# Optimization experiments

Hardware: AMD Instinct MI355X
Metric: run time of the kernel (lower is better)

Reference implementation:

```python
import jax, jax.numpy as jnp
import numpy as np


def _gaussian_splat_map(mask, sigma_x, sigma_y):
    """Equivalent to the torch scatter loop: for every pixel (p,q) with mask>0,
    add exp(-((i-p)^2/(2 sx^2) + (j-q)^2/(2 sy^2))) into map[b]. Because the
    Gaussian is separable, the sum over sources is exactly Gx @ M @ Gy with
    full HxH / WxW Gaussian distance kernels. Then normalize by per-batch max
    (max==0 -> 1)."""
    B, H, W = mask.shape
    ih = jnp.arange(H, dtype=jnp.float32)
    iw = jnp.arange(W, dtype=jnp.float32)
    dx = ih[:, None] - ih[None, :]                      # (H, H): i - p
    dy = iw[:, None] - iw[None, :]                      # (W, W): q - j (symmetric)
    Gx = jnp.exp(-(dx * dx) / (2.0 * sigma_x * sigma_x))
    Gy = jnp.exp(-(dy * dy) / (2.0 * sigma_y * sigma_y))
    m = (mask > 0).astype(jnp.float32)                  # (B, H, W) source indicator
    g = jnp.einsum('ip,bpq,qj->bij', Gx, m, Gy)         # summed Gaussians per batch
    mx = jnp.max(g, axis=(1, 2), keepdims=True)
    mx = jnp.where(mx == 0, jnp.float32(1.0), mx)
    return g / mx


def setup_inputs() -> dict:
    key = jax.random.key(0)
    B, C, H, W = 64, 4, 256, 256
    x = jax.random.normal(key, (B, C, H, W), dtype=jnp.float32)
    return {"x": x}


def reference(x):
    # x: (B, 4, H, W) -> output: (B, 5, H, W) with history=True, mul=True
    ch0 = x[:, 0, :, :]
    target = _gaussian_splat_map(x[:, 2, :, :], 1.0, 1.0)
    cost = _gaussian_splat_map(x[:, 1, :, :], 1.0, 1.0)
    hist = _gaussian_splat_map(x[:, 3, :, :], 0.5, 0.5)
    mul = target * cost
    return jnp.stack([ch0, target, cost, hist, mul], axis=1)
```

## Files before the change

kernel.cpp:

```cpp
#include <hip/hip_runtime.h>
#include <cmath>

#define HH 256
#define WW 256
#define BB 64
#define RR 4
#define OROWS 16
#define TROWS (OROWS + 2*RR)
#define TSTR 260

static __device__ __forceinline__ float bin(float v) { return (v > 0.0f) ? 1.0f : 0.0f; }

__global__ __launch_bounds__(256) void splat_kernel(const float* __restrict__ x,
                                                    float* __restrict__ out,
                                                    float* __restrict__ maxws) {
    __shared__ float tmp[TROWS * TSTR];
    __shared__ float wred[4];

    const int strip = blockIdx.x;
    const int z = blockIdx.y;
    const int b = z / 3;
    const int m = z - 3 * b;
    const int src_c = (m == 0) ? 2 : ((m == 1) ? 1 : 3);
    const float inv2s2 = (m == 2) ? 2.0f : 0.5f;

    float w[RR + 1];
#pragma unroll
    for (int d = 0; d <= RR; ++d) w[d] = expf(-(float)(d * d) * inv2s2);

    const int ti0 = strip * OROWS;
    const float* xc = x + (((size_t)b * 4 + src_c) << 16);
    const int tid = threadIdx.x;

#pragma unroll
    for (int t = 0; t < 3; ++t) {
        int idx = tid + t * 256;
        int r = idx >> 5;
        int g = idx & 31;
        int gi = ti0 + r - RR;
        float4 q0 = make_float4(0.f,0.f,0.f,0.f), q1 = q0, q2 = q0, q3 = q0;
        if (gi >= 0 && gi < HH) {
            const float4* row = (const float4*)(xc + ((size_t)gi << 8));
            int i0 = (g > 0) ? (2 * g - 1) : 0;
            int i3 = (g < 31) ? (2 * g + 2) : 63;
            q0 = row[i0];
            q1 = row[2 * g];
            q2 = row[2 * g + 1];
            q3 = row[i3];
            if (g == 0)  q0 = make_float4(0.f,0.f,0.f,0.f);
            if (g == 31) q3 = make_float4(0.f,0.f,0.f,0.f);
        }
        float a[16] = {bin(q0.x), bin(q0.y), bin(q0.z), bin(q0.w),
                       bin(q1.x), bin(q1.y), bin(q1.z), bin(q1.w),
                       bin(q2.x), bin(q2.y), bin(q2.z), bin(q2.w),
                       bin(q3.x), bin(q3.y), bin(q3.z), bin(q3.w)};
        float o[8];
#pragma unroll
        for (int j = 0; j < 8; ++j) {
            o[j] = w[4] * (a[j]     + a[j + 8])
                 + w[3] * (a[j + 1] + a[j + 7])
                 + w[2] * (a[j + 2] + a[j + 6])
                 + w[1] * (a[j + 3] + a[j + 5])
                 + w[0] *  a[j + 4];
        }
        float* trow = &tmp[r * TSTR + 8 * g];
        *(float4*)trow       = make_float4(o[0], o[1], o[2], o[3]);
        *(float4*)(trow + 4) = make_float4(o[4], o[5], o[6], o[7]);
    }
    __syncthreads();

    const int c = tid & 63;
    const int gr = tid >> 6;
    float4 acc[4];
#pragma unroll
    for (int rr = 0; rr < 4; ++rr) acc[rr] = make_float4(0.f,0.f,0.f,0.f);
#pragma unroll
    for (int k = 0; k < 12; ++k) {
        float4 v = *(const float4*)&tmp[(4 * gr + k) * TSTR + 4 * c];
#pragma unroll
        for (int rr = 0; rr < 4; ++rr) {
            int d = k - RR - rr;
            if (d >= -RR && d <= RR) {
                float wk = w[d < 0 ? -d : d];
                acc[rr].x += wk * v.x; acc[rr].y += wk * v.y;
                acc[rr].z += wk * v.z; acc[rr].w += wk * v.w;
            }
        }
    }

    float* oc = out + (((size_t)b * 5 + (m + 1)) << 16);
    float lmax = 0.0f;
#pragma unroll
    for (int rr = 0; rr < 4; ++rr) {
        int row = ti0 + 4 * gr + rr;
        *(float4*)&oc[((size_t)row << 8) + 4 * c] = acc[rr];
        lmax = fmaxf(lmax, fmaxf(fmaxf(acc[rr].x, acc[rr].y), fmaxf(acc[rr].z, acc[rr].w)));
    }

#pragma unroll
    for (int off = 32; off > 0; off >>= 1)
        lmax = fmaxf(lmax, __shfl_down(lmax, off, 64));
    if ((tid & 63) == 0) wred[tid >> 6] = lmax;
    __syncthreads();
    if (tid == 0)
        maxws[z * 16 + strip] = fmaxf(fmaxf(wred[0], wred[1]), fmaxf(wred[2], wred[3]));
}

__global__ __launch_bounds__(256) void finalize_kernel(const float* __restrict__ x,
                                                       float* __restrict__ out,
                                                       const float* __restrict__ maxws) {
    __shared__ float lds[48];
    const int b = blockIdx.x >> 3;
    const int slab = blockIdx.x & 7;
    const int tid = threadIdx.x;

    if (tid < 48) lds[tid] = maxws[b * 48 + tid];
    __syncthreads();

    float mt = 0.f, mc = 0.f, mh = 0.f;
#pragma unroll
    for (int s = 0; s < 16; ++s) {
        mt = fmaxf(mt, lds[s]);
        mc = fmaxf(mc, lds[16 + s]);
        mh = fmaxf(mh, lds[32 + s]);
    }
    if (mt == 0.f) mt = 1.f;
    if (mc == 0.f) mc = 1.f;
    if (mh == 0.f) mh = 1.f;
    const float rt = 1.f / mt, rc = 1.f / mc, rh = 1.f / mh;

    const int plane4 = HH * WW / 4;
    const float4* x0 = (const float4*)(x + ((size_t)b * 4 << 16));
    float4* o = (float4*)(out + ((size_t)b * 5 << 16));

#pragma unroll
    for (int i = 0; i < 8; ++i) {
        int q = slab * 2048 + i * 256 + tid;
        float4 c0 = x0[q];
        float4 t = o[plane4 + q];
        float4 c = o[2 * plane4 + q];
        float4 h = o[3 * plane4 + q];
        t.x *= rt; t.y *= rt; t.z *= rt; t.w *= rt;
        c.x *= rc; c.y *= rc; c.z *= rc; c.w *= rc;
        h.x *= rh; h.y *= rh; h.z *= rh; h.w *= rh;
        float4 mul = make_float4(t.x * c.x, t.y * c.y, t.z * c.z, t.w * c.w);
        o[q] = c0;
        o[plane4 + q] = t;
        o[2 * plane4 + q] = c;
        o[3 * plane4 + q] = h;
        o[4 * plane4 + q] = mul;
    }
}

extern "C" void kernel_launch(void* const* d_in, const int* in_sizes, int n_in,
                              void* d_out, int out_size, void* d_ws, size_t ws_size,
                              hipStream_t stream) {
    const float* x = (const float*)d_in[0];
    float* out = (float*)d_out;
    float* maxws = (float*)d_ws;

    dim3 g1(HH / OROWS, BB * 3);
    hipLaunchKernelGGL(splat_kernel, g1, dim3(256), 0, stream, x, out, maxws);

    hipLaunchKernelGGL(finalize_kernel, dim3(BB * 8), dim3(256), 0, stream, x, out, maxws);
}
```

Measured before the change: 154.9 us.

## Fuse splat and normalize into a cooperative persistent kernel with grid sync

Merges the splat and finalize kernels into one persistent cooperative kernel. Each block processes (batch, strip) units covering all three maps, copies channel 0 during phase 1, then waits on a grid-wide barrier and normalizes only its own strip in phase 2. The intent is to drop one launch and the per-map block split, and to touch freshly written output while it may still sit in cache. The cost is a grid sync, less parallelism per unit with the three maps serialized inside a block, and a two-kernel fallback path.

```diff
diff --git a/kernel.cpp b/kernel.cpp
--- a/kernel.cpp
+++ b/kernel.cpp
@@ -1,5 +1,8 @@
 #include <hip/hip_runtime.h>
+#include <hip/hip_cooperative_groups.h>
 #include <cmath>
+
+namespace cg = cooperative_groups;
 
 #define HH 256
 #define WW 256
@@ -8,148 +11,200 @@
 #define OROWS 16
 #define TROWS (OROWS + 2*RR)
 #define TSTR 260
+#define NUNITS (BB * 16)
 
 static __device__ __forceinline__ float bin(float v) { return (v > 0.0f) ? 1.0f : 0.0f; }
 
-__global__ __launch_bounds__(256) void splat_kernel(const float* __restrict__ x,
-                                                    float* __restrict__ out,
-                                                    float* __restrict__ maxws) {
-    __shared__ float tmp[TROWS * TSTR];
-    __shared__ float wred[4];
-
-    const int strip = blockIdx.x;
-    const int z = blockIdx.y;
-    const int b = z / 3;
-    const int m = z - 3 * b;
-    const int src_c = (m == 0) ? 2 : ((m == 1) ? 1 : 3);
-    const float inv2s2 = (m == 2) ? 2.0f : 0.5f;
-
-    float w[RR + 1];
-#pragma unroll
-    for (int d = 0; d <= RR; ++d) w[d] = expf(-(float)(d * d) * inv2s2);
-
+static __device__ __forceinline__ void unit_phase1(
+        int unit, int tid,
+        const float* __restrict__ x, float* __restrict__ out,
+        float* __restrict__ maxws, float* __restrict__ tmp,
+        float* __restrict__ wred) {
+    const int b = unit >> 4;
+    const int strip = unit & 15;
     const int ti0 = strip * OROWS;
-    const float* xc = x + (((size_t)b * 4 + src_c) << 16);
-    const int tid = threadIdx.x;
-
-#pragma unroll
-    for (int t = 0; t < 3; ++t) {
-        int idx = tid + t * 256;
-        int r = idx >> 5;
-        int g = idx & 31;
-        int gi = ti0 + r - RR;
-        float4 q0 = make_float4(0.f,0.f,0.f,0.f), q1 = q0, q2 = q0, q3 = q0;
-        if (gi >= 0 && gi < HH) {
-            const float4* row = (const float4*)(xc + ((size_t)gi << 8));
-            int i0 = (g > 0) ? (2 * g - 1) : 0;
-            int i3 = (g < 31) ? (2 * g + 2) : 63;
-            q0 = row[i0];
-            q1 = row[2 * g];
-            q2 = row[2 * g + 1];
-            q3 = row[i3];
-            if (g == 0)  q0 = make_float4(0.f,0.f,0.f,0.f);
-            if (g == 31) q3 = make_float4(0.f,0.f,0.f,0.f);
-        }
-        float a[16] = {bin(q0.x), bin(q0.y), bin(q0.z), bin(q0.w),
-                       bin(q1.x), bin(q1.y), bin(q1.z), bin(q1.w),
-                       bin(q2.x), bin(q2.y), bin(q2.z), bin(q2.w),
-                       bin(q3.x), bin(q3.y), bin(q3.z), bin(q3.w)};
-        float o[8];
-#pragma unroll
-        for (int j = 0; j < 8; ++j) {
-            o[j] = w[4] * (a[j]     + a[j + 8])
-                 + w[3] * (a[j + 1] + a[j + 7])
-                 + w[2] * (a[j + 2] + a[j + 6])
-                 + w[1] * (a[j + 3] + a[j + 5])
-                 + w[0] *  a[j + 4];
-        }
-        float* trow = &tmp[r * TSTR + 8 * g];
-        *(float4*)trow       = make_float4(o[0], o[1], o[2], o[3]);
-        *(float4*)(trow + 4) = make_float4(o[4], o[5], o[6], o[7]);
-    }
-    __syncthreads();
+
+    float w1[RR + 1], wh[RR + 1];
+#pragma unroll
+    for (int d = 0; d <= RR; ++d) {
+        w1[d] = __expf(-(float)(d * d) * 0.5f);
+        wh[d] = __expf(-(float)(d * d) * 2.0f);
+    }
+
+    {
+        const float4* x0 = (const float4*)(x + (((size_t)b << 2) << 16));
+        float4* o0 = (float4*)(out + (((size_t)b * 5) << 16));
+        const int base = ti0 << 6;
+#pragma unroll
+        for (int i = 0; i < 4; ++i) {
+            int q = base + (i << 8) + tid;
+            o0[q] = x0[q];
+        }
+    }
 
     const int c = tid & 63;
     const int gr = tid >> 6;
-    float4 acc[4];
-#pragma unroll
-    for (int rr = 0; rr < 4; ++rr) acc[rr] = make_float4(0.f,0.f,0.f,0.f);
-#pragma unroll
-    for (int k = 0; k < 12; ++k) {
-        float4 v = *(const float4*)&tmp[(4 * gr + k) * TSTR + 4 * c];
+
+#pragma unroll
+    for (int m = 0; m < 3; ++m) {
+        const int src_c = (m == 0) ? 2 : ((m == 1) ? 1 : 3);
+        const float* wm = (m == 2) ? wh : w1;
+        const float* xc = x + ((((size_t)b << 2) + src_c) << 16);
+
+#pragma unroll
+        for (int t = 0; t < 3; ++t) {
+            int idx = tid + t * 256;
+            int r = idx >> 5;
+            int g = idx & 31;
+            int gi = ti0 + r - RR;
+            float4 q0 = make_float4(0.f,0.f,0.f,0.f), q1 = q0, q2 = q0, q3 = q0;
+            if (gi >= 0 && gi < HH) {
+                const float4* row = (const float4*)(xc + ((size_t)gi << 8));
+                int i0 = (g > 0) ? (2 * g - 1) : 0;
+                int i3 = (g < 31) ? (2 * g + 2) : 63;
+                q0 = row[i0];
+                q1 = row[2 * g];
+                q2 = row[2 * g + 1];
+                q3 = row[i3];
+                if (g == 0)  q0 = make_float4(0.f,0.f,0.f,0.f);
+                if (g == 31) q3 = make_float4(0.f,0.f,0.f,0.f);
+            }
+            float a[16] = {bin(q0.x), bin(q0.y), bin(q0.z), bin(q0.w),
+                           bin(q1.x), bin(q1.y), bin(q1.z), bin(q1.w),
+                           bin(q2.x), bin(q2.y), bin(q2.z), bin(q2.w),
+                           bin(q3.x), bin(q3.y), bin(q3.z), bin(q3.w)};
+            float o[8];
+#pragma unroll
+            for (int j = 0; j < 8; ++j) {
+                o[j] = wm[4] * (a[j]     + a[j + 8])
+                     + wm[3] * (a[j + 1] + a[j + 7])
+                     + wm[2] * (a[j + 2] + a[j + 6])
+                     + wm[1] * (a[j + 3] + a[j + 5])
+                     + wm[0] *  a[j + 4];
+            }
+            float* trow = &tmp[r * TSTR + 8 * g];
+            *(float4*)trow       = make_float4(o[0], o[1], o[2], o[3]);
+            *(float4*)(trow + 4) = make_float4(o[4], o[5], o[6], o[7]);
+        }
+        __syncthreads();
+
+        float4 acc[4];
+#pragma unroll
+        for (int rr = 0; rr < 4; ++rr) acc[rr] = make_float4(0.f,0.f,0.f,0.f);
+#pragma unroll
+        for (int k = 0; k < 12; ++k) {
+            float4 v = *(const float4*)&tmp[(4 * gr + k) * TSTR + 4 * c];
+#pragma unroll
+            for (int rr = 0; rr < 4; ++rr) {
+                int d = k - RR - rr;
+                if (d >= -RR && d <= RR) {
+                    float wk = wm[d < 0 ? -d : d];
+                    acc[rr].x += wk * v.x; acc[rr].y += wk * v.y;
+                    acc[rr].z += wk * v.z; acc[rr].w += wk * v.w;
+                }
+            }
+        }
+
+        float* oc = out + (((size_t)b * 5 + (m + 1)) << 16);
+        float lmax = 0.0f;
 #pragma unroll
         for (int rr = 0; rr < 4; ++rr) {
-            int d = k - RR - rr;
-            if (d >= -RR && d <= RR) {
-                float wk = w[d < 0 ? -d : d];
-                acc[rr].x += wk * v.x; acc[rr].y += wk * v.y;
-                acc[rr].z += wk * v.z; acc[rr].w += wk * v.w;
-            }
-        }
-    }
-
-    float* oc = out + (((size_t)b * 5 + (m + 1)) << 16);
-    float lmax = 0.0f;
-#pragma unroll
-    for (int rr = 0; rr < 4; ++rr) {
-        int row = ti0 + 4 * gr + rr;
-        *(float4*)&oc[((size_t)row << 8) + 4 * c] = acc[rr];
-        lmax = fmaxf(lmax, fmaxf(fmaxf(acc[rr].x, acc[rr].y), fmaxf(acc[rr].z, acc[rr].w)));
-    }
-
-#pragma unroll
-    for (int off = 32; off > 0; off >>= 1)
-        lmax = fmaxf(lmax, __shfl_down(lmax, off, 64));
-    if ((tid & 63) == 0) wred[tid >> 6] = lmax;
+            int row = ti0 + 4 * gr + rr;
+            *(float4*)&oc[((size_t)row << 8) + 4 * c] = acc[rr];
+            lmax = fmaxf(lmax, fmaxf(fmaxf(acc[rr].x, acc[rr].y), fmaxf(acc[rr].z, acc[rr].w)));
+        }
+
+#pragma unroll
+        for (int off = 32; off > 0; off >>= 1)
+            lmax = fmaxf(lmax, __shfl_down(lmax, off, 64));
+        if (c == 0) wred[gr] = lmax;
+        __syncthreads();
+        if (tid == 0) {
+            float mx = fmaxf(fmaxf(wred[0], wred[1]), fmaxf(wred[2], wred[3]));
+            __hip_atomic_store(&maxws[b * 48 + m * 16 + strip], mx,
+                               __ATOMIC_RELAXED, __HIP_MEMORY_SCOPE_AGENT);
+        }
+        __syncthreads();
+    }
+}
+
+static __device__ __forceinline__ void unit_phase2(
+        int unit, int tid, float* __restrict__ out,
+        const float* __restrict__ maxws, float* __restrict__ smax) {
+    const int b = unit >> 4;
+    const int strip = unit & 15;
+    const int ti0 = strip * OROWS;
+
+    if (tid < 48)
+        smax[tid] = __hip_atomic_load(&maxws[b * 48 + tid],
+                                      __ATOMIC_RELAXED, __HIP_MEMORY_SCOPE_AGENT);
     __syncthreads();
-    if (tid == 0)
-        maxws[z * 16 + strip] = fmaxf(fmaxf(wred[0], wred[1]), fmaxf(wred[2], wred[3]));
-}
-
-__global__ __launch_bounds__(256) void finalize_kernel(const float* __restrict__ x,
-                                                       float* __restrict__ out,
-                                                       const float* __restrict__ maxws) {
-    __shared__ float lds[48];
-    const int b = blockIdx.x >> 3;
-    const int slab = blockIdx.x & 7;
-    const int tid = threadIdx.x;
-
-    if (tid < 48) lds[tid] = maxws[b * 48 + tid];
-    __syncthreads();
 
     float mt = 0.f, mc = 0.f, mh = 0.f;
 #pragma unroll
     for (int s = 0; s < 16; ++s) {
-        mt = fmaxf(mt, lds[s]);
-        mc = fmaxf(mc, lds[16 + s]);
-        mh = fmaxf(mh, lds[32 + s]);
+        mt = fmaxf(mt, smax[s]);
+        mc = fmaxf(mc, smax[16 + s]);
+        mh = fmaxf(mh, smax[32 + s]);
     }
     if (mt == 0.f) mt = 1.f;
     if (mc == 0.f) mc = 1.f;
     if (mh == 0.f) mh = 1.f;
     const float rt = 1.f / mt, rc = 1.f / mc, rh = 1.f / mh;
 
-    const int plane4 = HH * WW / 4;
-    const float4* x0 = (const float4*)(x + ((size_t)b * 4 << 16));
-    float4* o = (float4*)(out + ((size_t)b * 5 << 16));
-
-#pragma unroll
-    for (int i = 0; i < 8; ++i) {
-        int q = slab * 2048 + i * 256 + tid;
-        float4 c0 = x0[q];
-        float4 t = o[plane4 + q];
-        float4 c = o[2 * plane4 + q];
-        float4 h = o[3 * plane4 + q];
-        t.x *= rt; t.y *= rt; t.z *= rt; t.w *= rt;
-        c.x *= rc; c.y *= rc; c.z *= rc; c.w *= rc;
-        h.x *= rh; h.y *= rh; h.z *= rh; h.w *= rh;
-        float4 mul = make_float4(t.x * c.x, t.y * c.y, t.z * c.z, t.w * c.w);
-        o[q] = c0;
-        o[plane4 + q] = t;
-        o[2 * plane4 + q] = c;
-        o[3 * plane4 + q] = h;
-        o[4 * plane4 + q] = mul;
-    }
+    float4* o1 = (float4*)(out + (((size_t)b * 5 + 1) << 16));
+    float4* o2 = (float4*)(out + (((size_t)b * 5 + 2) << 16));
+    float4* o3 = (float4*)(out + (((size_t)b * 5 + 3) << 16));
+    float4* o4 = (float4*)(out + (((size_t)b * 5 + 4) << 16));
+    const int base = ti0 << 6;
+#pragma unroll
+    for (int i = 0; i < 4; ++i) {
+        int q = base + (i << 8) + tid;
+        float4 t = o1[q], cc = o2[q], h = o3[q];
+        t.x *= rt;  t.y *= rt;  t.z *= rt;  t.w *= rt;
+        cc.x *= rc; cc.y *= rc; cc.z *= rc; cc.w *= rc;
+        h.x *= rh;  h.y *= rh;  h.z *= rh;  h.w *= rh;
+        float4 mul = make_float4(t.x * cc.x, t.y * cc.y, t.z * cc.z, t.w * cc.w);
+        o1[q] = t;
+        o2[q] = cc;
+        o3[q] = h;
+        o4[q] = mul;
+    }
+    __syncthreads();
+}
+
+__global__ __launch_bounds__(256, 4) void fused_kernel(const float* __restrict__ x,
+                                                       float* __restrict__ out,
+                                                       float* __restrict__ maxws) {
+    __shared__ float tmp[TROWS * TSTR];
+    __shared__ float wred[4];
+    __shared__ float smax[48];
+
+    const int tid = threadIdx.x;
+    const int G = gridDim.x;
+    const int bid = (blockIdx.x & 7) * (G >> 3) + (blockIdx.x >> 3);
+
+    for (int u = bid; u < NUNITS; u += G)
+        unit_phase1(u, tid, x, out, maxws, tmp, wred);
+
+    cg::this_grid().sync();
+
+    for (int u = bid; u < NUNITS; u += G)
+        unit_phase2(u, tid, out, maxws, smax);
+}
+
+__global__ __launch_bounds__(256) void phase1_kernel(const float* __restrict__ x,
+                                                     float* __restrict__ out,
+                                                     float* __restrict__ maxws) {
+    __shared__ float tmp[TROWS * TSTR];
+    __shared__ float wred[4];
+    unit_phase1(blockIdx.x, threadIdx.x, x, out, maxws, tmp, wred);
+}
+
+__global__ __launch_bounds__(256) void phase2_kernel(float* __restrict__ out,
+                                                     const float* __restrict__ maxws) {
+    __shared__ float smax[48];
+    unit_phase2(blockIdx.x, threadIdx.x, out, maxws, smax);
 }
 
 extern "C" void kernel_launch(void* const* d_in, const int* in_sizes, int n_in,
@@ -159,8 +214,33 @@
     float* out = (float*)d_out;
     float* maxws = (float*)d_ws;
 
-    dim3 g1(HH / OROWS, BB * 3);
-    hipLaunchKernelGGL(splat_kernel, g1, dim3(256), 0, stream, x, out, maxws);
-
-    hipLaunchKernelGGL(finalize_kernel, dim3(BB * 8), dim3(256), 0, stream, x, out, maxws);
-}
+    static int G = -2;
+    if (G == -2) {
+        G = -1;
+        hipDeviceProp_t prop{};
+        int dev = 0;
+        if (hipGetDevice(&dev) == hipSuccess &&
+            hipGetDeviceProperties(&prop, dev) == hipSuccess &&
+            prop.cooperativeLaunch) {
+            int maxb = 0;
+            if (hipOccupancyMaxActiveBlocksPerMultiprocessor(
+                    &maxb, (const void*)fused_kernel, 256, 0) == hipSuccess && maxb > 0) {
+                long lim = (long)maxb * (long)prop.multiProcessorCount;
+                long g = (lim < (long)NUNITS) ? lim : (long)NUNITS;
+                g = (g / 8) * 8;
+                if (g >= 8) G = (int)g;
+            }
+        }
+    }
+
+    if (G > 0) {
+        void* args[] = { (void*)&x, (void*)&out, (void*)&maxws };
+        if (hipLaunchCooperativeKernel((const void*)fused_kernel, dim3(G), dim3(256),
+                                       args, 0, stream) == hipSuccess)
+            return;
+        G = -1;
+    }
+
+    hipLaunchKernelGGL(phase1_kernel, dim3(NUNITS), dim3(256), 0, stream, x, out, maxws);
+    hipLaunchKernelGGL(phase2_kernel, dim3(NUNITS), dim3(256), 0, stream, out, maxws);
+}
```

Measured after the change: 231.8 us. 1.5x slower.

## Fuse splat and normalize into one kernel with per-batch grid barrier

Applied to the files above, without the earlier changes.

Merges the splat and finalize kernels into one persistent-style kernel. Each block computes all three maps for its strip, keeps the results in registers packed to bf16-like 16-bit halves, and accumulates per-batch maxima with atomicMax. Blocks of a batch then wait on a counter spin barrier before normalizing and writing all outputs. This removes the intermediate write and readback of three planes, and it risks deadlock if not all 16 strips of a batch are co-resident. Truncating values to 16 bits also loses precision.

```diff
diff --git a/kernel.cpp b/kernel.cpp
--- a/kernel.cpp
+++ b/kernel.cpp
@@ -8,147 +8,164 @@
 #define OROWS 16
 #define TROWS (OROWS + 2*RR)
 #define TSTR 260
+#define NUNITS (BB * 16)
 
 static __device__ __forceinline__ float bin(float v) { return (v > 0.0f) ? 1.0f : 0.0f; }
+static __device__ __forceinline__ unsigned pk2(float a, float b) {
+    return (__float_as_uint(a) >> 16) | (__float_as_uint(b) & 0xffff0000u);
+}
+static __device__ __forceinline__ float up_lo(unsigned u) { return __uint_as_float(u << 16); }
+static __device__ __forceinline__ float up_hi(unsigned u) { return __uint_as_float(u & 0xffff0000u); }
 
-__global__ __launch_bounds__(256) void splat_kernel(const float* __restrict__ x,
-                                                    float* __restrict__ out,
-                                                    float* __restrict__ maxws) {
+__global__ __launch_bounds__(256, 5) void fused_kernel(const float* __restrict__ x,
+                                                       float* __restrict__ out,
+                                                       int* __restrict__ ws) {
     __shared__ float tmp[TROWS * TSTR];
-    __shared__ float wred[4];
 
-    const int strip = blockIdx.x;
-    const int z = blockIdx.y;
-    const int b = z / 3;
-    const int m = z - 3 * b;
-    const int src_c = (m == 0) ? 2 : ((m == 1) ? 1 : 3);
-    const float inv2s2 = (m == 2) ? 2.0f : 0.5f;
+    int* bmax = ws;
+    int* cnt  = ws + 192;
 
-    float w[RR + 1];
+    const int bid = blockIdx.x;
+    const int unit = (bid & 7) * (NUNITS >> 3) + (bid >> 3);
+    const int b = unit >> 4;
+    const int strip = unit & 15;
+    const int ti0 = strip * OROWS;
+    const int tid = threadIdx.x;
+    const int c = tid & 63;
+    const int gr = tid >> 6;
+
+    {
+        const float4* x0 = (const float4*)(x + (((size_t)b << 2) << 16));
+        float4* o0 = (float4*)(out + (((size_t)b * 5) << 16));
+        const int base = ti0 << 6;
 #pragma unroll
-    for (int d = 0; d <= RR; ++d) w[d] = expf(-(float)(d * d) * inv2s2);
+        for (int i = 0; i < 4; ++i) {
+            int q = base + (i << 8) + tid;
+            o0[q] = x0[q];
+        }
+    }
 
-    const int ti0 = strip * OROWS;
-    const float* xc = x + (((size_t)b * 4 + src_c) << 16);
-    const int tid = threadIdx.x;
+    unsigned pkm[3][8];
 
 #pragma unroll
-    for (int t = 0; t < 3; ++t) {
-        int idx = tid + t * 256;
-        int r = idx >> 5;
-        int g = idx & 31;
-        int gi = ti0 + r - RR;
-        float4 q0 = make_float4(0.f,0.f,0.f,0.f), q1 = q0, q2 = q0, q3 = q0;
-        if (gi >= 0 && gi < HH) {
-            const float4* row = (const float4*)(xc + ((size_t)gi << 8));
-            int i0 = (g > 0) ? (2 * g - 1) : 0;
-            int i3 = (g < 31) ? (2 * g + 2) : 63;
-            q0 = row[i0];
-            q1 = row[2 * g];
-            q2 = row[2 * g + 1];
-            q3 = row[i3];
-            if (g == 0)  q0 = make_float4(0.f,0.f,0.f,0.f);
-            if (g == 31) q3 = make_float4(0.f,0.f,0.f,0.f);
+    for (int m = 0; m < 3; ++m) {
+        const int src_c = (m == 0) ? 2 : ((m == 1) ? 1 : 3);
+        const float inv2s2 = (m == 2) ? 2.0f : 0.5f;
+        const float* xc = x + ((((size_t)b << 2) + src_c) << 16);
+
+        float wm[RR + 1];
+#pragma unroll
+        for (int d = 0; d <= RR; ++d) wm[d] = __expf(-(float)(d * d) * inv2s2);
+
+#pragma unroll
+        for (int t = 0; t < 3; ++t) {
+            int idx = tid + t * 256;
+            int r = idx >> 5;
+            int g = idx & 31;
+            int gi = ti0 + r - RR;
+            float4 q0 = make_float4(0.f,0.f,0.f,0.f), q1 = q0, q2 = q0, q3 = q0;
+            if (gi >= 0 && gi < HH) {
+                const float4* row = (const float4*)(xc + ((size_t)gi << 8));
+                int i0 = (g > 0) ? (2 * g - 1) : 0;
+                int i3 = (g < 31) ? (2 * g + 2) : 63;
+                q0 = row[i0];
+                q1 = row[2 * g];
+                q2 = row[2 * g + 1];
+                q3 = row[i3];
+                if (g == 0)  q0 = make_float4(0.f,0.f,0.f,0.f);
+                if (g == 31) q3 = make_float4(0.f,0.f,0.f,0.f);
+            }
+            float a[16] = {bin(q0.x), bin(q0.y), bin(q0.z), bin(q0.w),
+                           bin(q1.x), bin(q1.y), bin(q1.z), bin(q1.w),
+                           bin(q2.x), bin(q2.y), bin(q2.z), bin(q2.w),
+                           bin(q3.x), bin(q3.y), bin(q3.z), bin(q3.w)};
+            float o[8];
+#pragma unroll
+            for (int j = 0; j < 8; ++j) {
+                o[j] = wm[4] * (a[j]     + a[j + 8])
+                     + wm[3] * (a[j + 1] + a[j + 7])
+                     + wm[2] * (a[j + 2] + a[j + 6])
+                     + wm[1] * (a[j + 3] + a[j + 5])
+                     + wm[0] *  a[j + 4];
+            }
+            float* trow = &tmp[r * TSTR + 8 * g];
+            *(float4*)trow       = make_float4(o[0], o[1], o[2], o[3]);
+            *(float4*)(trow + 4) = make_float4(o[4], o[5], o[6], o[7]);
         }
-        float a[16] = {bin(q0.x), bin(q0.y), bin(q0.z), bin(q0.w),
-                       bin(q1.x), bin(q1.y), bin(q1.z), bin(q1.w),
-                       bin(q2.x), bin(q2.y), bin(q2.z), bin(q2.w),
-                       bin(q3.x), bin(q3.y), bin(q3.z), bin(q3.w)};
-        float o[8];
+        __syncthreads();
+
+        float4 acc[4];
 #pragma unroll
-        for (int j = 0; j < 8; ++j) {
-            o[j] = w[4] * (a[j]     + a[j + 8])
-                 + w[3] * (a[j + 1] + a[j + 7])
-                 + w[2] * (a[j + 2] + a[j + 6])
-                 + w[1] * (a[j + 3] + a[j + 5])
-                 + w[0] *  a[j + 4];
+        for (int rr = 0; rr < 4; ++rr) acc[rr] = make_float4(0.f,0.f,0.f,0.f);
+#pragma unroll
+        for (int k = 0; k < 12; ++k) {
+            float4 v = *(const float4*)&tmp[(4 * gr + k) * TSTR + 4 * c];
+#pragma unroll
+            for (int rr = 0; rr < 4; ++rr) {
+                int d = k - RR - rr;
+                if (d >= -RR && d <= RR) {
+                    float wk = wm[d < 0 ? -d : d];
+                    acc[rr].x += wk * v.x; acc[rr].y += wk * v.y;
+                    acc[rr].z += wk * v.z; acc[rr].w += wk * v.w;
+                }
+            }
         }
-        float* trow = &tmp[r * TSTR + 8 * g];
-        *(float4*)trow       = make_float4(o[0], o[1], o[2], o[3]);
-        *(float4*)(trow + 4) = make_float4(o[4], o[5], o[6], o[7]);
+
+        float lmax = 0.0f;
+#pragma unroll
+        for (int rr = 0; rr < 4; ++rr) {
+            pkm[m][2 * rr]     = pk2(acc[rr].x, acc[rr].y);
+            pkm[m][2 * rr + 1] = pk2(acc[rr].z, acc[rr].w);
+            lmax = fmaxf(lmax, fmaxf(fmaxf(acc[rr].x, acc[rr].y), fmaxf(acc[rr].z, acc[rr].w)));
+        }
+#pragma unroll
+        for (int off = 32; off > 0; off >>= 1)
+            lmax = fmaxf(lmax, __shfl_down(lmax, off, 64));
+        if (c == 0) atomicMax(&bmax[b * 3 + m], __float_as_int(lmax));
+
+        __syncthreads();
+    }
+
+    if (tid == 0) {
+        __hip_atomic_fetch_add(&cnt[b], 1, __ATOMIC_ACQ_REL, __HIP_MEMORY_SCOPE_AGENT);
+        while (__hip_atomic_load(&cnt[b], __ATOMIC_ACQUIRE, __HIP_MEMORY_SCOPE_AGENT) < 16)
+            __builtin_amdgcn_s_sleep(2);
     }
     __syncthreads();
 
-    const int c = tid & 63;
-    const int gr = tid >> 6;
-    float4 acc[4];
-#pragma unroll
-    for (int rr = 0; rr < 4; ++rr) acc[rr] = make_float4(0.f,0.f,0.f,0.f);
-#pragma unroll
-    for (int k = 0; k < 12; ++k) {
-        float4 v = *(const float4*)&tmp[(4 * gr + k) * TSTR + 4 * c];
-#pragma unroll
-        for (int rr = 0; rr < 4; ++rr) {
-            int d = k - RR - rr;
-            if (d >= -RR && d <= RR) {
-                float wk = w[d < 0 ? -d : d];
-                acc[rr].x += wk * v.x; acc[rr].y += wk * v.y;
-                acc[rr].z += wk * v.z; acc[rr].w += wk * v.w;
-            }
-        }
-    }
-
-    float* oc = out + (((size_t)b * 5 + (m + 1)) << 16);
-    float lmax = 0.0f;
-#pragma unroll
-    for (int rr = 0; rr < 4; ++rr) {
-        int row = ti0 + 4 * gr + rr;
-        *(float4*)&oc[((size_t)row << 8) + 4 * c] = acc[rr];
-        lmax = fmaxf(lmax, fmaxf(fmaxf(acc[rr].x, acc[rr].y), fmaxf(acc[rr].z, acc[rr].w)));
-    }
-
-#pragma unroll
-    for (int off = 32; off > 0; off >>= 1)
-        lmax = fmaxf(lmax, __shfl_down(lmax, off, 64));
-    if ((tid & 63) == 0) wred[tid >> 6] = lmax;
-    __syncthreads();
-    if (tid == 0)
-        maxws[z * 16 + strip] = fmaxf(fmaxf(wred[0], wred[1]), fmaxf(wred[2], wred[3]));
-}
-
-__global__ __launch_bounds__(256) void finalize_kernel(const float* __restrict__ x,
-                                                       float* __restrict__ out,
-                                                       const float* __restrict__ maxws) {
-    __shared__ float lds[48];
-    const int b = blockIdx.x >> 3;
-    const int slab = blockIdx.x & 7;
-    const int tid = threadIdx.x;
-
-    if (tid < 48) lds[tid] = maxws[b * 48 + tid];
-    __syncthreads();
-
-    float mt = 0.f, mc = 0.f, mh = 0.f;
-#pragma unroll
-    for (int s = 0; s < 16; ++s) {
-        mt = fmaxf(mt, lds[s]);
-        mc = fmaxf(mc, lds[16 + s]);
-        mh = fmaxf(mh, lds[32 + s]);
-    }
+    float mt = __int_as_float(__hip_atomic_load(&bmax[b * 3 + 0], __ATOMIC_RELAXED,
+                                                __HIP_MEMORY_SCOPE_AGENT));
+    float mc = __int_as_float(__hip_atomic_load(&bmax[b * 3 + 1], __ATOMIC_RELAXED,
+                                                __HIP_MEMORY_SCOPE_AGENT));
+    float mh = __int_as_float(__hip_atomic_load(&bmax[b * 3 + 2], __ATOMIC_RELAXED,
+                                                __HIP_MEMORY_SCOPE_AGENT));
     if (mt == 0.f) mt = 1.f;
     if (mc == 0.f) mc = 1.f;
     if (mh == 0.f) mh = 1.f;
     const float rt = 1.f / mt, rc = 1.f / mc, rh = 1.f / mh;
 
-    const int plane4 = HH * WW / 4;
-    const float4* x0 = (const float4*)(x + ((size_t)b * 4 << 16));
-    float4* o = (float4*)(out + ((size_t)b * 5 << 16));
-
+    float* o1 = out + (((size_t)b * 5 + 1) << 16);
+    float* o2 = out + (((size_t)b * 5 + 2) << 16);
+    float* o3 = out + (((size_t)b * 5 + 3) << 16);
+    float* o4 = out + (((size_t)b * 5 + 4) << 16);
 #pragma unroll
-    for (int i = 0; i < 8; ++i) {
-        int q = slab * 2048 + i * 256 + tid;
-        float4 c0 = x0[q];
-        float4 t = o[plane4 + q];
-        float4 c = o[2 * plane4 + q];
-        float4 h = o[3 * plane4 + q];
-        t.x *= rt; t.y *= rt; t.z *= rt; t.w *= rt;
-        c.x *= rc; c.y *= rc; c.z *= rc; c.w *= rc;
-        h.x *= rh; h.y *= rh; h.z *= rh; h.w *= rh;
-        float4 mul = make_float4(t.x * c.x, t.y * c.y, t.z * c.z, t.w * c.w);
-        o[q] = c0;
-        o[plane4 + q] = t;
-        o[2 * plane4 + q] = c;
-        o[3 * plane4 + q] = h;
-        o[4 * plane4 + q] = mul;
+    for (int rr = 0; rr < 4; ++rr) {
+        const int row = ti0 + 4 * gr + rr;
+        const size_t off = ((size_t)row << 8) + 4 * c;
+        unsigned t01 = pkm[0][2 * rr], t23 = pkm[0][2 * rr + 1];
+        unsigned c01 = pkm[1][2 * rr], c23 = pkm[1][2 * rr + 1];
+        unsigned h01 = pkm[2][2 * rr], h23 = pkm[2][2 * rr + 1];
+        float4 t  = make_float4(up_lo(t01) * rt, up_hi(t01) * rt,
+                                up_lo(t23) * rt, up_hi(t23) * rt);
+        float4 cc = make_float4(up_lo(c01) * rc, up_hi(c01) * rc,
+                                up_lo(c23) * rc, up_hi(c23) * rc);
+        float4 h  = make_float4(up_lo(h01) * rh, up_hi(h01) * rh,
+                                up_lo(h23) * rh, up_hi(h23) * rh);
+        float4 mul = make_float4(t.x * cc.x, t.y * cc.y, t.z * cc.z, t.w * cc.w);
+        *(float4*)&o1[off] = t;
+        *(float4*)&o2[off] = cc;
+        *(float4*)&o3[off] = h;
+        *(float4*)&o4[off] = mul;
     }
 }
 
@@ -157,10 +174,8 @@
                               hipStream_t stream) {
     const float* x = (const float*)d_in[0];
     float* out = (float*)d_out;
-    float* maxws = (float*)d_ws;
+    int* ws = (int*)d_ws;
 
-    dim3 g1(HH / OROWS, BB * 3);
-    hipLaunchKernelGGL(splat_kernel, g1, dim3(256), 0, stream, x, out, maxws);
-
-    hipLaunchKernelGGL(finalize_kernel, dim3(BB * 8), dim3(256), 0, stream, x, out, maxws);
+    hipMemsetAsync(d_ws, 0, 1024, stream);
+    hipLaunchKernelGGL(fused_kernel, dim3(NUNITS), dim3(256), 0, stream, x, out, ws);
 }
```

Result: slower. 207.7 us (+34.1%).

## Store intermediate splat maps as truncated bf16 in workspace and move channel-0 copy

Applied to the files above, without the earlier changes.

The splat kernel now writes unnormalized maps to a workspace as packed bf16 (truncated upper halves) instead of fp32 into the output. The finalize kernel reads these half-size maps instead of re-reading fp32 output planes, which cuts intermediate memory traffic. The channel-0 copy moves into the splat kernel's m==0 blocks, and the Gaussian weights now use __expf. Truncating to bf16 loses precision in the final maps, which risks exceeding tolerance. An fp32 fallback path runs when the workspace is too small, so whether the new path runs depends on the workspace size the harness provides.

```diff
diff --git a/kernel.cpp b/kernel.cpp
--- a/kernel.cpp
+++ b/kernel.cpp
@@ -9,11 +9,21 @@
 #define TROWS (OROWS + 2*RR)
 #define TSTR 260
 
+#define MAPS_U32 ((size_t)192 * 32768)
+#define NEED_WS  (MAPS_U32 * 4 + 192 * 16 * 4)
+
 static __device__ __forceinline__ float bin(float v) { return (v > 0.0f) ? 1.0f : 0.0f; }
-
-__global__ __launch_bounds__(256) void splat_kernel(const float* __restrict__ x,
-                                                    float* __restrict__ out,
-                                                    float* __restrict__ maxws) {
+static __device__ __forceinline__ unsigned pk2(float a, float b) {
+    return (__float_as_uint(a) >> 16) | (__float_as_uint(b) & 0xffff0000u);
+}
+static __device__ __forceinline__ float up_lo(unsigned u) { return __uint_as_float(u << 16); }
+static __device__ __forceinline__ float up_hi(unsigned u) { return __uint_as_float(u & 0xffff0000u); }
+
+
+__global__ __launch_bounds__(256) void splat_bf16(const float* __restrict__ x,
+                                                  float* __restrict__ out,
+                                                  unsigned* __restrict__ wsmaps,
+                                                  float* __restrict__ maxws) {
     __shared__ float tmp[TROWS * TSTR];
     __shared__ float wred[4];
 
@@ -26,11 +36,22 @@
 
     float w[RR + 1];
 #pragma unroll
-    for (int d = 0; d <= RR; ++d) w[d] = expf(-(float)(d * d) * inv2s2);
+    for (int d = 0; d <= RR; ++d) w[d] = __expf(-(float)(d * d) * inv2s2);
 
     const int ti0 = strip * OROWS;
     const float* xc = x + (((size_t)b * 4 + src_c) << 16);
     const int tid = threadIdx.x;
+
+    if (m == 0) {
+        const float4* x0 = (const float4*)(x + (((size_t)b * 4) << 16));
+        float4* o0 = (float4*)(out + (((size_t)b * 5) << 16));
+        const int base = ti0 << 6;
+#pragma unroll
+        for (int i = 0; i < 4; ++i) {
+            int q = base + i * 256 + tid;
+            o0[q] = x0[q];
+        }
+    }
 
 #pragma unroll
     for (int t = 0; t < 3; ++t) {
@@ -88,6 +109,140 @@
         }
     }
 
+    unsigned* wz = wsmaps + ((size_t)z << 15);
+    float lmax = 0.0f;
+#pragma unroll
+    for (int rr = 0; rr < 4; ++rr) {
+        int row = ti0 + 4 * gr + rr;
+        *(uint2*)&wz[row * 128 + 2 * c] = make_uint2(pk2(acc[rr].x, acc[rr].y),
+                                                     pk2(acc[rr].z, acc[rr].w));
+        lmax = fmaxf(lmax, fmaxf(fmaxf(acc[rr].x, acc[rr].y), fmaxf(acc[rr].z, acc[rr].w)));
+    }
+
+#pragma unroll
+    for (int off = 32; off > 0; off >>= 1)
+        lmax = fmaxf(lmax, __shfl_down(lmax, off, 64));
+    if ((tid & 63) == 0) wred[tid >> 6] = lmax;
+    __syncthreads();
+    if (tid == 0)
+        maxws[z * 16 + strip] = fmaxf(fmaxf(wred[0], wred[1]), fmaxf(wred[2], wred[3]));
+}
+
+__global__ __launch_bounds__(256) void finalize_bf16(const unsigned* __restrict__ wsmaps,
+                                                     const float* __restrict__ maxws,
+                                                     float* __restrict__ out) {
+    __shared__ float lds[48];
+    const int b = blockIdx.x >> 3;
+    const int slab = blockIdx.x & 7;
+    const int tid = threadIdx.x;
+
+    if (tid < 48) lds[tid] = maxws[b * 48 + tid];
+    __syncthreads();
+
+    float mt = 0.f, mc = 0.f, mh = 0.f;
+#pragma unroll
+    for (int s = 0; s < 16; ++s) {
+        mt = fmaxf(mt, lds[s]);
+        mc = fmaxf(mc, lds[16 + s]);
+        mh = fmaxf(mh, lds[32 + s]);
+    }
+    if (mt == 0.f) mt = 1.f;
+    if (mc == 0.f) mc = 1.f;
+    if (mh == 0.f) mh = 1.f;
+    const float rt = 1.f / mt, rc = 1.f / mc, rh = 1.f / mh;
+
+    const int plane4 = HH * WW / 4;
+    const unsigned* zt = wsmaps + ((size_t)(b * 3 + 0) << 15);
+    const unsigned* zc = wsmaps + ((size_t)(b * 3 + 1) << 15);
+    const unsigned* zh = wsmaps + ((size_t)(b * 3 + 2) << 15);
+    float4* o = (float4*)(out + (((size_t)b * 5) << 16));
+
+#pragma unroll
+    for (int i = 0; i < 8; ++i) {
+        int q = slab * 2048 + i * 256 + tid;
+        uint2 tu = *(const uint2*)&zt[2 * q];
+        uint2 cu = *(const uint2*)&zc[2 * q];
+        uint2 hu = *(const uint2*)&zh[2 * q];
+        float4 t = make_float4(up_lo(tu.x) * rt, up_hi(tu.x) * rt,
+                               up_lo(tu.y) * rt, up_hi(tu.y) * rt);
+        float4 cc = make_float4(up_lo(cu.x) * rc, up_hi(cu.x) * rc,
+                                up_lo(cu.y) * rc, up_hi(cu.y) * rc);
+        float4 h = make_float4(up_lo(hu.x) * rh, up_hi(hu.x) * rh,
+                               up_lo(hu.y) * rh, up_hi(hu.y) * rh);
+        float4 mul = make_float4(t.x * cc.x, t.y * cc.y, t.z * cc.z, t.w * cc.w);
+        o[plane4 + q] = t;
+        o[2 * plane4 + q] = cc;
+        o[3 * plane4 + q] = h;
+        o[4 * plane4 + q] = mul;
+    }
+}
+
+__global__ __launch_bounds__(256) void splat_f32(const float* __restrict__ x,
+                                                 float* __restrict__ out,
+                                                 float* __restrict__ maxws) {
+    __shared__ float tmp[TROWS * TSTR];
+    __shared__ float wred[4];
+    const int strip = blockIdx.x;
+    const int z = blockIdx.y;
+    const int b = z / 3;
+    const int m = z - 3 * b;
+    const int src_c = (m == 0) ? 2 : ((m == 1) ? 1 : 3);
+    const float inv2s2 = (m == 2) ? 2.0f : 0.5f;
+    float w[RR + 1];
+#pragma unroll
+    for (int d = 0; d <= RR; ++d) w[d] = __expf(-(float)(d * d) * inv2s2);
+    const int ti0 = strip * OROWS;
+    const float* xc = x + (((size_t)b * 4 + src_c) << 16);
+    const int tid = threadIdx.x;
+#pragma unroll
+    for (int t = 0; t < 3; ++t) {
+        int idx = tid + t * 256;
+        int r = idx >> 5;
+        int g = idx & 31;
+        int gi = ti0 + r - RR;
+        float4 q0 = make_float4(0.f,0.f,0.f,0.f), q1 = q0, q2 = q0, q3 = q0;
+        if (gi >= 0 && gi < HH) {
+            const float4* row = (const float4*)(xc + ((size_t)gi << 8));
+            int i0 = (g > 0) ? (2 * g - 1) : 0;
+            int i3 = (g < 31) ? (2 * g + 2) : 63;
+            q0 = row[i0]; q1 = row[2 * g]; q2 = row[2 * g + 1]; q3 = row[i3];
+            if (g == 0)  q0 = make_float4(0.f,0.f,0.f,0.f);
+            if (g == 31) q3 = make_float4(0.f,0.f,0.f,0.f);
+        }
+        float a[16] = {bin(q0.x), bin(q0.y), bin(q0.z), bin(q0.w),
+                       bin(q1.x), bin(q1.y), bin(q1.z), bin(q1.w),
+                       bin(q2.x), bin(q2.y), bin(q2.z), bin(q2.w),
+                       bin(q3.x), bin(q3.y), bin(q3.z), bin(q3.w)};
+        float o[8];
+#pragma unroll
+        for (int j = 0; j < 8; ++j) {
+            o[j] = w[4] * (a[j] + a[j + 8]) + w[3] * (a[j + 1] + a[j + 7])
+                 + w[2] * (a[j + 2] + a[j + 6]) + w[1] * (a[j + 3] + a[j + 5])
+                 + w[0] * a[j + 4];
+        }
+        float* trow = &tmp[r * TSTR + 8 * g];
+        *(float4*)trow       = make_float4(o[0], o[1], o[2], o[3]);
+        *(float4*)(trow + 4) = make_float4(o[4], o[5], o[6], o[7]);
+    }
+    __syncthreads();
+    const int c = tid & 63;
+    const int gr = tid >> 6;
+    float4 acc[4];
+#pragma unroll
+    for (int rr = 0; rr < 4; ++rr) acc[rr] = make_float4(0.f,0.f,0.f,0.f);
+#pragma unroll
+    for (int k = 0; k < 12; ++k) {
+        float4 v = *(const float4*)&tmp[(4 * gr + k) * TSTR + 4 * c];
+#pragma unroll
+        for (int rr = 0; rr < 4; ++rr) {
+            int d = k - RR - rr;
+            if (d >= -RR && d <= RR) {
+                float wk = w[d < 0 ? -d : d];
+                acc[rr].x += wk * v.x; acc[rr].y += wk * v.y;
+                acc[rr].z += wk * v.z; acc[rr].w += wk * v.w;
+            }
+        }
+    }
     float* oc = out + (((size_t)b * 5 + (m + 1)) << 16);
     float lmax = 0.0f;
 #pragma unroll
@@ -96,7 +251,6 @@
         *(float4*)&oc[((size_t)row << 8) + 4 * c] = acc[rr];
         lmax = fmaxf(lmax, fmaxf(fmaxf(acc[rr].x, acc[rr].y), fmaxf(acc[rr].z, acc[rr].w)));
     }
-
 #pragma unroll
     for (int off = 32; off > 0; off >>= 1)
         lmax = fmaxf(lmax, __shfl_down(lmax, off, 64));
@@ -106,17 +260,15 @@
         maxws[z * 16 + strip] = fmaxf(fmaxf(wred[0], wred[1]), fmaxf(wred[2], wred[3]));
 }
 
-__global__ __launch_bounds__(256) void finalize_kernel(const float* __restrict__ x,
-                                                       float* __restrict__ out,
-                                                       const float* __restrict__ maxws) {
+__global__ __launch_bounds__(256) void finalize_f32(const float* __restrict__ x,
+                                                    float* __restrict__ out,
+                                                    const float* __restrict__ maxws) {
     __shared__ float lds[48];
     const int b = blockIdx.x >> 3;
     const int slab = blockIdx.x & 7;
     const int tid = threadIdx.x;
-
     if (tid < 48) lds[tid] = maxws[b * 48 + tid];
     __syncthreads();
-
     float mt = 0.f, mc = 0.f, mh = 0.f;
 #pragma unroll
     for (int s = 0; s < 16; ++s) {
@@ -128,11 +280,9 @@
     if (mc == 0.f) mc = 1.f;
     if (mh == 0.f) mh = 1.f;
     const float rt = 1.f / mt, rc = 1.f / mc, rh = 1.f / mh;
-
     const int plane4 = HH * WW / 4;
     const float4* x0 = (const float4*)(x + ((size_t)b * 4 << 16));
     float4* o = (float4*)(out + ((size_t)b * 5 << 16));
-
 #pragma unroll
     for (int i = 0; i < 8; ++i) {
         int q = slab * 2048 + i * 256 + tid;
@@ -157,10 +307,19 @@
                               hipStream_t stream) {
     const float* x = (const float*)d_in[0];
     float* out = (float*)d_out;
-    float* maxws = (float*)d_ws;
-
-    dim3 g1(HH / OROWS, BB * 3);
-    hipLaunchKernelGGL(splat_kernel, g1, dim3(256), 0, stream, x, out, maxws);
-
-    hipLaunchKernelGGL(finalize_kernel, dim3(BB * 8), dim3(256), 0, stream, x, out, maxws);
-}
+
+    if (ws_size >= NEED_WS) {
+        unsigned* wsmaps = (unsigned*)d_ws;
+        float* maxws = (float*)d_ws + MAPS_U32;
+        hipLaunchKernelGGL(splat_bf16, dim3(16, 192), dim3(256), 0, stream,
+                           x, out, wsmaps, maxws);
+        hipLaunchKernelGGL(finalize_bf16, dim3(BB * 8), dim3(256), 0, stream,
+                           wsmaps, maxws, out);
+    } else {
+        float* maxws = (float*)d_ws;
+        hipLaunchKernelGGL(splat_f32, dim3(16, 192), dim3(256), 0, stream,
+                           x, out, maxws);
+        hipLaunchKernelGGL(finalize_f32, dim3(BB * 8), dim3(256), 0, stream,
+                           x, out, maxws);
+    }
+}
```

Measured after the change: 142.4 us. -8.0%, faster.
